# Performance work log

Hardware: AMD Instinct MI355X
Metric: run time of the kernel (lower is better)

The kernel has to match this reference:

```python
import jax, jax.numpy as jnp
import numpy as np

B, T, N, SD, D, HYP, EMB = 128, 256, 8, 200, 64, 64, 32

def _ln(x, g, b, eps=1e-5):
    mu = jnp.mean(x, -1, keepdims=True)
    v = jnp.mean((x - mu) ** 2, -1, keepdims=True)
    return (x - mu) * jax.lax.rsqrt(v + eps) * g + b

def setup_inputs():
    key = jax.random.key(0)
    ks = iter(jax.random.split(key, 64))
    def p(shape, scale=0.05):
        return (jax.random.normal(next(ks), shape) * scale).astype(jnp.float32)
    n, sd, d, hyp, emb = N, SD, D, HYP, EMB
    return dict(
        qvals=p((B, T, n), 1.0), states=p((B, T, sd), 1.0), hidden_state=p((B, T, n, d), 1.0),
        enc_w1=p((sd, d)), enc_b1=p((d,)), enc_w2=p((d, d)), enc_b2=p((d,)),
        wq=p((d, d)), bq=p((d,)), wk=p((d, d)), bk=p((d,)), wv=p((d, d)), bv=p((d,)),
        wo=p((d, d)), bo=p((d,)),
        ln1_g=jnp.ones((d,), jnp.float32), ln1_b=jnp.zeros((d,), jnp.float32),
        ffn_w1=p((d, d)), ffn_b1=p((d,)), ffn_w2=p((d, d)), ffn_b2=p((d,)),
        ln2_g=jnp.ones((d,), jnp.float32), ln2_b=jnp.zeros((d,), jnp.float32),
        fc2ni_w=p((n, d, n - 1)), fc2ni_b=p((n, n - 1)),
        norm_g=jnp.ones((n - 1,), jnp.float32), norm_b=jnp.zeros((n - 1,), jnp.float32),
        w1a=p((2 * d, hyp)), b1a=p((hyp,)), w1b=p((hyp, n * emb)), b1b=p((n * emb,)),
        hb1w=p((2 * d, emb)), hb1b=p((emb,)),
        w2a=p((2 * d, hyp)), b2a=p((hyp,)), w2b=p((hyp, emb)), b2b=p((emb,)),
        hb2w1=p((2 * d, emb)), hb2b1=p((emb,)), hb2w2=p((emb, 1)), hb2b2=p((1,)))

def reference(qvals, states, hidden_state, enc_w1, enc_b1, enc_w2, enc_b2,
              wq, bq, wk, bk, wv, bv, wo, bo, ln1_g, ln1_b,
              ffn_w1, ffn_b1, ffn_w2, ffn_b2, ln2_g, ln2_b,
              fc2ni_w, fc2ni_b, norm_g, norm_b,
              w1a, b1a, w1b, b1b, hb1w, hb1b,
              w2a, b2a, w2b, b2b, hb2w1, hb2b1, hb2w2, hb2b2):
    sg = jax.lax.stop_gradient
    b, t, n = qvals.shape
    bt = b * t
    d = hidden_state.shape[-1]
    emb = hb1w.shape[1]
    # Encoder_s: relu(fc1) then tanh(fc2(e)+e)
    s = states.reshape(bt, -1)
    e = jax.nn.relu(s @ enc_w1 + enc_b1)
    enc = jnp.tanh(e @ enc_w2 + enc_b2 + e)                       # (bt, 64)
    # concat detached agent hiddens with detached state embedding -> (bt, n+1, 64)
    h = jnp.concatenate([sg(hidden_state.reshape(bt, n, d)), sg(enc)[:, None, :]], axis=1)
    # transformer block (single-head self-attention + FFN, post-LN)
    q = h @ wq + bq; k = h @ wk + bk; v = h @ wv + bv
    att = jax.nn.softmax(jnp.einsum('bid,bjd->bij', q, k) / jnp.sqrt(jnp.float32(d)), axis=-1)
    h2 = _ln(h + (att @ v) @ wo + bo, ln1_g, ln1_b)
    h3 = _ln(h2 + jax.nn.relu(h2 @ ffn_w1 + ffn_b1) @ ffn_w2 + ffn_b2, ln2_g, ln2_b)
    h_trans = h3[:, :n]                                           # (bt, n, 64)
    ens = jnp.concatenate([enc, sg(h_trans).mean(1)], axis=-1)    # (bt, 128)
    # per-agent fc2_Ni -> LayerNorm -> sigmoid, vectorized over agents
    ni = jnp.einsum('xnd,nde->xne', h_trans, fc2ni_w) + fc2ni_b   # (bt, n, n-1)
    ni = jax.nn.sigmoid(_ln(ni, norm_g, norm_b))
    # insert 1.0 at the diagonal (agent i keeps its own q with weight 1)
    rows = jnp.arange(n)[:, None]; cols = jnp.arange(n)[None, :]
    gidx = jnp.clip(cols - (cols > rows).astype(jnp.int32), 0, n - 2)  # (n, n)
    gathered = jnp.take_along_axis(ni, jnp.broadcast_to(gidx, (bt, n, n)), axis=-1)
    nfull = jnp.where(cols == rows, jnp.float32(1.0), gathered)   # (bt, n, n)
    N_nn = nfull.reshape(b, t, n, n)
    q_ni = (qvals[:, :, None, :] * N_nn).sum(-1).reshape(bt, 1, n)
    # hypernetwork mixing (QMIX)
    ens_d = sg(ens)
    w1 = jnp.abs(jax.nn.relu(ens_d @ w1a + b1a) @ w1b + b1b).reshape(bt, n, emb)
    b1 = (ens_d @ hb1w + hb1b).reshape(bt, 1, emb)
    w2 = jnp.abs(jax.nn.relu(ens @ w2a + b2a) @ w2b + b2b).reshape(bt, emb, 1)
    b2 = (jax.nn.relu(ens @ hb2w1 + hb2b1) @ hb2w2 + hb2b2).reshape(bt, 1, 1)
    hidden = jax.nn.elu(q_ni @ w1 + b1)
    y = (hidden @ w2 + b2).reshape(b, t, 1)
    eye_mask = jnp.broadcast_to(jnp.eye(n, dtype=bool), (b, t, n, n))
    return y, N_nn, eye_mask
```

## Files before the change

### kernel.cpp

```cpp
#include <hip/hip_runtime.h>
#include <hip/hip_bf16.h>

typedef __bf16 bf16x8 __attribute__((ext_vector_type(8)));
typedef __bf16 bf16x4 __attribute__((ext_vector_type(4)));
typedef float f32x4 __attribute__((ext_vector_type(4)));

#define ROWSG 32768
#define RB 8
#define HPAD 72
#define NN_OFF ((size_t)ROWSG)
#define EYE_OFF ((size_t)ROWSG + (size_t)ROWSG*64)

#define OFF_EW1   0
#define OFF_EW2   14336
#define OFF_WQ    18432
#define OFF_WK    22528
#define OFF_WV    26624
#define OFF_WO    30720
#define OFF_F1    34816
#define OFF_F2    38912
#define OFF_W1A   43008
#define OFF_W1B   51200
#define OFF_HB1W  67584
#define OFF_W2A   71680
#define OFF_W2B   79872
#define OFF_HB2W1 81920
#define WS_TOTAL  86016

__device__ __align__(16) __bf16 g_ws[WS_TOTAL];

#define MFMA16(a,b,c) __builtin_amdgcn_mfma_f32_16x16x32_bf16(a,b,c,0,0,0)

struct TP { const float* src[14]; };

__global__ __launch_bounds__(256) void wtrans(TP tp) {
    const int gid = blockIdx.x * 256 + threadIdx.x;
    if (gid >= WS_TOTAL) return;
    const int OFFS[14] = {OFF_EW1, OFF_EW2, OFF_WQ, OFF_WK, OFF_WV, OFF_WO, OFF_F1,
                          OFF_F2, OFF_W1A, OFF_W1B, OFF_HB1W, OFF_W2A, OFF_W2B, OFF_HB2W1};
    const int KPS[14]  = {224, 64, 64, 64, 64, 64, 64, 64, 128, 64, 128, 128, 64, 128};
    const int KRS[14]  = {200, 64, 64, 64, 64, 64, 64, 64, 128, 64, 128, 128, 64, 128};
    const int NS[14]   = {64, 64, 64, 64, 64, 64, 64, 64, 64, 256, 32, 64, 32, 32};
    int m = 0;
#pragma unroll
    for (int i = 1; i < 14; ++i) if (gid >= OFFS[i]) m = i;
    const int loc = gid - OFFS[m];
    const int Kp = KPS[m];
    const int n = loc / Kp;
    const int k = loc - n * Kp;
    float v = 0.f;
    if (k < KRS[m]) v = tp.src[m][(size_t)k * NS[m] + n];
    g_ws[gid] = (__bf16)v;
}

struct MainP {
    const float *qvals, *states, *hid, *eb1, *eb2, *bq, *bk, *bv, *bo,
        *l1g, *l1b, *fb1, *fb2, *l2g, *l2b, *niw, *nib, *ng, *nb,
        *b1a, *b1b, *hb1b, *b2a, *b2b, *hb2b1, *hw2, *hb2b2;
    float* out;
};

__device__ __forceinline__ void proj_ln(const __bf16* A, const __bf16* WT,
                                        const float* bias, const float* g, const float* bb,
                                        __bf16* H, int w, int quad, int l15) {
    for (int mti = 0; mti < 2; ++mti) {
        const int mt = w + 4 * mti;
        if (mt >= 5) continue;
        f32x4 acc0 = {0,0,0,0}, acc1 = {0,0,0,0}, acc2 = {0,0,0,0}, acc3 = {0,0,0,0};
#pragma unroll
        for (int ks = 0; ks < 2; ++ks) {
            const int kk = ks * 32 + quad * 8;
            const bf16x8 af = *(const bf16x8*)(A + (mt * 16 + l15) * HPAD + kk);
            acc0 = MFMA16(af, *(const bf16x8*)(WT + (size_t)(0 * 16 + l15) * 64 + kk), acc0);
            acc1 = MFMA16(af, *(const bf16x8*)(WT + (size_t)(1 * 16 + l15) * 64 + kk), acc1);
            acc2 = MFMA16(af, *(const bf16x8*)(WT + (size_t)(2 * 16 + l15) * 64 + kk), acc2);
            acc3 = MFMA16(af, *(const bf16x8*)(WT + (size_t)(3 * 16 + l15) * 64 + kk), acc3);
        }
        float v[4][4], g4[4], b4[4];
#pragma unroll
        for (int nt = 0; nt < 4; ++nt) {
            const int col = nt * 16 + l15;
            const float bo = bias[col];
            g4[nt] = g[col]; b4[nt] = bb[col];
            const f32x4 a = (nt == 0) ? acc0 : (nt == 1) ? acc1 : (nt == 2) ? acc2 : acc3;
#pragma unroll
            for (int r = 0; r < 4; ++r)
                v[nt][r] = a[r] + bo + (float)H[(mt * 16 + quad * 4 + r) * HPAD + col];
        }
#pragma unroll
        for (int r = 0; r < 4; ++r) {
            float s  = v[0][r] + v[1][r] + v[2][r] + v[3][r];
            float s2 = v[0][r]*v[0][r] + v[1][r]*v[1][r] + v[2][r]*v[2][r] + v[3][r]*v[3][r];
#pragma unroll
            for (int off = 1; off < 16; off <<= 1) {
                s  += __shfl_xor(s,  off, 64);
                s2 += __shfl_xor(s2, off, 64);
            }
            const float mu  = s * 0.015625f;
            const float var = s2 * 0.015625f - mu * mu;
            const float rs  = rsqrtf(var + 1e-5f);
#pragma unroll
            for (int nt = 0; nt < 4; ++nt)
                H[(mt * 16 + quad * 4 + r) * HPAD + nt * 16 + l15] =
                    (__bf16)((v[nt][r] - mu) * rs * g4[nt] + b4[nt]);
        }
    }
}

__global__ __launch_bounds__(256) void mixer_main(MainP p) {
    __shared__ __align__(16) __bf16 Hb[80 * HPAD];
    __shared__ __align__(16) __bf16 Qb[80 * HPAD];
    __shared__ __align__(16) __bf16 Kb[80 * HPAD];
    __shared__ __align__(16) __bf16 EbU[16 * HPAD];
    __shared__ __align__(16) __bf16 Tb2[16 * HPAD];
    __shared__ __align__(16) __bf16 ensB[16 * 136];
    __shared__ float  attU[8 * 81];
    __shared__ float  sQv[64];
    __shared__ float  qniL[64];
    __shared__ __align__(16) __bf16 W1bS[8 * 256];
    __shared__ float  B1f[8 * 32], W2f[8 * 32], T3f[8 * 32];

    const int blk = blockIdx.x;
    const int bt0 = blk * RB;
    const int t = threadIdx.x;
    const int w = t >> 6, lane = t & 63, quad = lane >> 4, l15 = lane & 15;
    const __bf16* ws = g_ws;
    __bf16* Sb = W1bS;

#pragma unroll
    for (int it = 0; it < 4; ++it) {
        const int u = it * 256 + t;
        const int x = u >> 7, rem = u & 127, n = rem >> 4, d4 = (rem & 15) * 4;
        const float4 v4 = *(const float4*)(p.hid + ((size_t)(bt0 + x) * 512 + n * 64 + d4));
        bf16x4 o; o[0] = (__bf16)v4.x; o[1] = (__bf16)v4.y; o[2] = (__bf16)v4.z; o[3] = (__bf16)v4.w;
        *(bf16x4*)(Hb + (x * 9 + n) * HPAD + d4) = o;
    }
#pragma unroll
    for (int it = 0; it < 2; ++it) {
        const int u = it * 256 + t;
        if (u < 400) {
            const int xr = u / 50, c4 = u - xr * 50;
            const float4 v4 = *(const float4*)(p.states + (size_t)(bt0 + xr) * 200 + c4 * 4);
            bf16x4 o; o[0] = (__bf16)v4.x; o[1] = (__bf16)v4.y; o[2] = (__bf16)v4.z; o[3] = (__bf16)v4.w;
            *(bf16x4*)(Sb + xr * 224 + c4 * 4) = o;
        }
    }
    if (t < 192) { const int xr = t / 24, c = t - xr * 24; Sb[xr * 224 + 200 + c] = (__bf16)0.0f; }
    if (t < 64) sQv[t] = p.qvals[(size_t)(bt0 + (t >> 3)) * 8 + (t & 7)];
    __syncthreads();

    float e4[4];
    {
        const int n0 = w * 16;
        const int srow = (l15 < 8) ? l15 : 7;
        f32x4 acc = {0, 0, 0, 0};
        for (int ks = 0; ks < 7; ++ks) {
            const int kk = ks * 32 + quad * 8;
            const bf16x8 af = *(const bf16x8*)(Sb + srow * 224 + kk);
            const bf16x8 bf = *(const bf16x8*)(ws + OFF_EW1 + (size_t)(n0 + l15) * 224 + kk);
            acc = MFMA16(af, bf, acc);
        }
        const float b1 = p.eb1[n0 + l15];
#pragma unroll
        for (int r = 0; r < 4; ++r) {
            const float ev = fmaxf(acc[r] + b1, 0.f);
            e4[r] = ev;
            EbU[(quad * 4 + r) * HPAD + n0 + l15] = (__bf16)ev;
        }
    }
    __syncthreads();

    {
        const int n0 = w * 16;
        f32x4 acc = {0, 0, 0, 0};
#pragma unroll
        for (int ks = 0; ks < 2; ++ks) {
            const int kk = ks * 32 + quad * 8;
            const bf16x8 af = *(const bf16x8*)(EbU + l15 * HPAD + kk);
            const bf16x8 bf = *(const bf16x8*)(ws + OFF_EW2 + (size_t)(n0 + l15) * 64 + kk);
            acc = MFMA16(af, bf, acc);
        }
        const float b2 = p.eb2[n0 + l15];
#pragma unroll
        for (int r = 0; r < 4; ++r) {
            const int xr = quad * 4 + r;
            if (xr < RB) {
                const float ev = tanhf(acc[r] + e4[r] + b2);
                Hb[(xr * 9 + 8) * HPAD + n0 + l15] = (__bf16)ev;
                ensB[xr * 136 + n0 + l15] = (__bf16)ev;
            }
        }
    }
    __syncthreads();

    for (int it = 0; it < 10; ++it) {
        const int j = w + 4 * it;
        const int mat = j / 20, r20 = j % 20, mt = r20 >> 2, nt = r20 & 3;
        const __bf16* wt = ws + (mat == 0 ? OFF_WQ : OFF_WK);
        const float* bias = (mat == 0 ? p.bq : p.bk);
        __bf16* dst = (mat == 0 ? Qb : Kb);
        f32x4 acc = {0, 0, 0, 0};
#pragma unroll
        for (int ks = 0; ks < 2; ++ks) {
            const int kk = ks * 32 + quad * 8;
            const bf16x8 af = *(const bf16x8*)(Hb + (mt * 16 + l15) * HPAD + kk);
            const bf16x8 bf = *(const bf16x8*)(wt + (size_t)(nt * 16 + l15) * 64 + kk);
            acc = MFMA16(af, bf, acc);
        }
        const float bv = bias[nt * 16 + l15];
#pragma unroll
        for (int r = 0; r < 4; ++r)
            dst[(mt * 16 + quad * 4 + r) * HPAD + nt * 16 + l15] = (__bf16)(acc[r] + bv);
    }
    __syncthreads();

    for (int xi = 0; xi < 2; ++xi) {
        const int x = w * 2 + xi;
        const int arow = (x * 9 + l15) * HPAD;
        f32x4 acc = {0, 0, 0, 0};
#pragma unroll
        for (int ks = 0; ks < 2; ++ks) {
            const int kk = ks * 32 + quad * 8;
            const bf16x8 qa = *(const bf16x8*)(Qb + arow + kk);
            const bf16x8 kb = *(const bf16x8*)(Kb + arow + kk);
            acc = MFMA16(qa, kb, acc);
        }
#pragma unroll
        for (int r = 0; r < 4; ++r) {
            const int i = quad * 4 + r;
            float s = (l15 < 9) ? acc[r] * 0.125f : -3.0e38f;
            float m = s;
#pragma unroll
            for (int off = 1; off < 16; off <<= 1) m = fmaxf(m, __shfl_xor(m, off, 64));
            float e = (l15 < 9) ? __expf(s - m) : 0.f;
            float sum = e;
#pragma unroll
            for (int off = 1; off < 16; off <<= 1) sum += __shfl_xor(sum, off, 64);
            const float pv = e / sum;
            if (i < 9 && l15 < 9) attU[x * 81 + i * 9 + l15] = pv;
        }
    }
    __syncthreads();

    for (int xi = 0; xi < 2; ++xi) {
        const int x = w * 2 + xi;
        float vreg[9];
#pragma unroll
        for (int jj = 0; jj < 9; ++jj) vreg[jj] = (float)Hb[(x * 9 + jj) * HPAD + lane];
#pragma unroll
        for (int i = 0; i < 9; ++i) {
            float a = 0.f;
#pragma unroll
            for (int jj = 0; jj < 9; ++jj) a += attU[x * 81 + i * 9 + jj] * vreg[jj];
            Kb[(x * 9 + i) * HPAD + lane] = (__bf16)a;
        }
    }
    __syncthreads();

    for (int it = 0; it < 5; ++it) {
        const int j = w + 4 * it;
        const int mt = j >> 2, nt = j & 3;
        f32x4 acc = {0, 0, 0, 0};
#pragma unroll
        for (int ks = 0; ks < 2; ++ks) {
            const int kk = ks * 32 + quad * 8;
            const bf16x8 af = *(const bf16x8*)(Kb + (mt * 16 + l15) * HPAD + kk);
            const bf16x8 bf = *(const bf16x8*)(ws + OFF_WV + (size_t)(nt * 16 + l15) * 64 + kk);
            acc = MFMA16(af, bf, acc);
        }
        const float bv = p.bv[nt * 16 + l15];
#pragma unroll
        for (int r = 0; r < 4; ++r)
            Qb[(mt * 16 + quad * 4 + r) * HPAD + nt * 16 + l15] = (__bf16)(acc[r] + bv);
    }
    __syncthreads();

    proj_ln(Qb, ws + OFF_WO, p.bo, p.l1g, p.l1b, Hb, w, quad, l15);
    __syncthreads();

    for (int it = 0; it < 5; ++it) {
        const int j = w + 4 * it;
        const int mt = j >> 2, nt = j & 3;
        f32x4 acc = {0, 0, 0, 0};
#pragma unroll
        for (int ks = 0; ks < 2; ++ks) {
            const int kk = ks * 32 + quad * 8;
            const bf16x8 af = *(const bf16x8*)(Hb + (mt * 16 + l15) * HPAD + kk);
            const bf16x8 bf = *(const bf16x8*)(ws + OFF_F1 + (size_t)(nt * 16 + l15) * 64 + kk);
            acc = MFMA16(af, bf, acc);
        }
        const float fb = p.fb1[nt * 16 + l15];
#pragma unroll
        for (int r = 0; r < 4; ++r)
            Kb[(mt * 16 + quad * 4 + r) * HPAD + nt * 16 + l15] = (__bf16)fmaxf(acc[r] + fb, 0.f);
    }
    __syncthreads();

    proj_ln(Kb, ws + OFF_F2, p.fb2, p.l2g, p.l2b, Hb, w, quad, l15);
    __syncthreads();

#pragma unroll
    for (int it = 0; it < 2; ++it) {
        const int id = it * 256 + t;
        const int x = id >> 6, col = id & 63;
        float s = 0.f;
#pragma unroll
        for (int i = 0; i < 8; ++i) s += (float)Hb[(x * 9 + i) * HPAD + col];
        ensB[x * 136 + 64 + col] = (__bf16)(s * 0.125f);
    }
    __syncthreads();

    {
        const int pr = t >> 2, q4 = t & 3;
        const int x = pr >> 3, n = pr & 7;
        float acc[7] = {0.f, 0.f, 0.f, 0.f, 0.f, 0.f, 0.f};
        const float* wni = p.niw + n * 448;
        for (int dd = 0; dd < 16; ++dd) {
            const int d = q4 * 16 + dd;
            const float hv = (float)Hb[(x * 9 + n) * HPAD + d];
#pragma unroll
            for (int e = 0; e < 7; ++e) acc[e] += hv * wni[d * 7 + e];
        }
#pragma unroll
        for (int e = 0; e < 7; ++e) {
            acc[e] += __shfl_xor(acc[e], 1, 64);
            acc[e] += __shfl_xor(acc[e], 2, 64);
        }
        if (q4 == 0) {
            float s = 0.f;
#pragma unroll
            for (int e = 0; e < 7; ++e) { acc[e] += p.nib[n * 7 + e]; s += acc[e]; }
            const float mu = s * (1.f / 7.f);
            float s2 = 0.f;
#pragma unroll
            for (int e = 0; e < 7; ++e) { const float d0 = acc[e] - mu; s2 += d0 * d0; }
            const float rs = rsqrtf(s2 * (1.f / 7.f) + 1e-5f);
            float* sNi = (float*)EbU;
#pragma unroll
            for (int e = 0; e < 7; ++e) {
                const float vv = (acc[e] - mu) * rs * p.ng[e] + p.nb[e];
                sNi[x * 64 + n * 8 + e] = 1.f / (1.f + __expf(-vv));
            }
        }
    }
    __syncthreads();

    {
        const float* sNi = (const float*)EbU;
        float* Nf = attU;
#pragma unroll
        for (int it = 0; it < 2; ++it) {
            const int id = it * 256 + t;
            const int x = id >> 6, rem = id & 63, i = rem >> 3, jj = rem & 7;
            const float nf = (i == jj) ? 1.f : sNi[x * 64 + i * 8 + (jj - (jj > i ? 1 : 0))];
            p.out[NN_OFF + (size_t)(bt0 + x) * 64 + rem] = nf;
            p.out[EYE_OFF + (size_t)(bt0 + x) * 64 + rem] = (i == jj) ? 1.f : 0.f;
            Nf[x * 64 + rem] = nf;
        }
    }
    __syncthreads();
    {
        const float* Nf = attU;
        const int pr = t >> 2, q4 = t & 3;
        const int x = pr >> 3, i = pr & 7;
        const int j0 = q4 * 2;
        float s = sQv[x * 8 + j0] * Nf[x * 64 + i * 8 + j0] +
                  sQv[x * 8 + j0 + 1] * Nf[x * 64 + i * 8 + j0 + 1];
        s += __shfl_xor(s, 1, 64);
        s += __shfl_xor(s, 2, 64);
        if (q4 == 0) qniL[x * 8 + i] = s;
    }
    __syncthreads();

    {
        const int n0 = w * 16;
#pragma unroll
        for (int m2 = 0; m2 < 2; ++m2) {
            const __bf16* wt = ws + (m2 == 0 ? OFF_W1A : OFF_W2A);
            const float* bias = m2 == 0 ? p.b1a : p.b2a;
            __bf16* dst = m2 == 0 ? EbU : Tb2;
            f32x4 acc = {0, 0, 0, 0};
#pragma unroll
            for (int ks = 0; ks < 4; ++ks) {
                const int kk = ks * 32 + quad * 8;
                const bf16x8 af = *(const bf16x8*)(ensB + l15 * 136 + kk);
                const bf16x8 bf = *(const bf16x8*)(wt + (size_t)(n0 + l15) * 128 + kk);
                acc = MFMA16(af, bf, acc);
            }
            const float bb = bias[n0 + l15];
#pragma unroll
            for (int r = 0; r < 4; ++r)
                dst[(quad * 4 + r) * HPAD + n0 + l15] = (__bf16)fmaxf(acc[r] + bb, 0.f);
        }
    }
    __syncthreads();

    for (int it = 0; it < 6; ++it) {
        const int j = w + 4 * it;
        if (j >= 22) continue;
        int mode, n0, Kp, ksteps, aStride;
        const __bf16 *A, *WT; const float* bias;
        if (j < 16)      { mode = 0; n0 = j * 16;        A = EbU;  aStride = HPAD; WT = ws + OFF_W1B;   bias = p.b1b;  Kp = 64;  ksteps = 2; }
        else if (j < 18) { mode = 1; n0 = (j - 16) * 16; A = ensB; aStride = 136;  WT = ws + OFF_HB1W;  bias = p.hb1b; Kp = 128; ksteps = 4; }
        else if (j < 20) { mode = 2; n0 = (j - 18) * 16; A = Tb2;  aStride = HPAD; WT = ws + OFF_W2B;   bias = p.b2b;  Kp = 64;  ksteps = 2; }
        else             { mode = 3; n0 = (j - 20) * 16; A = ensB; aStride = 136;  WT = ws + OFF_HB2W1; bias = p.hb2b1;Kp = 128; ksteps = 4; }
        f32x4 acc = {0, 0, 0, 0};
        for (int ks = 0; ks < ksteps; ++ks) {
            const int kk = ks * 32 + quad * 8;
            const bf16x8 af = *(const bf16x8*)(A + l15 * aStride + kk);
            const bf16x8 bf = *(const bf16x8*)(WT + (size_t)(n0 + l15) * Kp + kk);
            acc = MFMA16(af, bf, acc);
        }
        const float bb = bias[n0 + l15];
#pragma unroll
        for (int r = 0; r < 4; ++r) {
            const int xr = quad * 4 + r;
            if (xr < RB) {
                const float val = acc[r] + bb;
                if (mode == 0)      W1bS[xr * 256 + n0 + l15] = (__bf16)fabsf(val);
                else if (mode == 1) B1f[xr * 32 + n0 + l15] = val;
                else if (mode == 2) W2f[xr * 32 + n0 + l15] = fabsf(val);
                else                T3f[xr * 32 + n0 + l15] = fmaxf(val, 0.f);
            }
        }
    }
    __syncthreads();

    if (t < 128) {
        const int x = t >> 4, sub = t & 15;
        float pp = 0.f, pb = 0.f;
#pragma unroll
        for (int h2i = 0; h2i < 2; ++h2i) {
            const int e = sub + h2i * 16;
            float a = B1f[x * 32 + e];
#pragma unroll
            for (int i = 0; i < 8; ++i) a += qniL[x * 8 + i] * (float)W1bS[x * 256 + i * 32 + e];
            const float hid = a > 0.f ? a : (__expf(a) - 1.f);
            pp += hid * W2f[x * 32 + e];
            pb += T3f[x * 32 + e] * p.hw2[e];
        }
#pragma unroll
        for (int off = 1; off < 16; off <<= 1) {
            pp += __shfl_xor(pp, off, 64);
            pb += __shfl_xor(pb, off, 64);
        }
        if (sub == 0) p.out[bt0 + x] = pp + pb + p.hb2b2[0];
    }
}

extern "C" void kernel_launch(void* const* d_in, const int* in_sizes, int n_in,
                              void* d_out, int out_size, void* d_ws, size_t ws_size,
                              hipStream_t stream) {
    TP tp;
    tp.src[0]  = (const float*)d_in[3];
    tp.src[1]  = (const float*)d_in[5];
    tp.src[2]  = (const float*)d_in[7];
    tp.src[3]  = (const float*)d_in[9];
    tp.src[4]  = (const float*)d_in[11];
    tp.src[5]  = (const float*)d_in[13];
    tp.src[6]  = (const float*)d_in[17];
    tp.src[7]  = (const float*)d_in[19];
    tp.src[8]  = (const float*)d_in[27];
    tp.src[9]  = (const float*)d_in[29];
    tp.src[10] = (const float*)d_in[31];
    tp.src[11] = (const float*)d_in[33];
    tp.src[12] = (const float*)d_in[35];
    tp.src[13] = (const float*)d_in[37];
    wtrans<<<(WS_TOTAL + 255) / 256, 256, 0, stream>>>(tp);

    MainP p;
    p.qvals = (const float*)d_in[0];
    p.states = (const float*)d_in[1];
    p.hid = (const float*)d_in[2];
    p.eb1 = (const float*)d_in[4];
    p.eb2 = (const float*)d_in[6];
    p.bq = (const float*)d_in[8];
    p.bk = (const float*)d_in[10];
    p.bv = (const float*)d_in[12];
    p.bo = (const float*)d_in[14];
    p.l1g = (const float*)d_in[15];
    p.l1b = (const float*)d_in[16];
    p.fb1 = (const float*)d_in[18];
    p.fb2 = (const float*)d_in[20];
    p.l2g = (const float*)d_in[21];
    p.l2b = (const float*)d_in[22];
    p.niw = (const float*)d_in[23];
    p.nib = (const float*)d_in[24];
    p.ng = (const float*)d_in[25];
    p.nb = (const float*)d_in[26];
    p.b1a = (const float*)d_in[28];
    p.b1b = (const float*)d_in[30];
    p.hb1b = (const float*)d_in[32];
    p.b2a = (const float*)d_in[34];
    p.b2b = (const float*)d_in[36];
    p.hb2b1 = (const float*)d_in[38];
    p.hw2 = (const float*)d_in[39];
    p.hb2b2 = (const float*)d_in[40];
    p.out = (float*)d_out;

    mixer_main<<<ROWSG / RB, 256, 0, stream>>>(p);
}
```

Before: 430.8 us.

## Give each wavefront its own rows and LDS slice to drop block barriers

Restructures the fused mixer kernel so each of the four wavefronts processes two batch-time rows independently in a private 8 KB LDS slice, removing all block-wide __syncthreads. Per-row work (attention over 9 tokens, FFN, layer norms, hypernetwork heads) now uses MFMA tiles with only 9 of 16 rows valid, trading wasted MFMA lanes for no inter-wave synchronisation. It also cuts shared memory and adds a launch bound of 4 blocks per CU to raise occupancy. The risks are lower MFMA utilisation, since more tiles are padded, and weight reloads now happen per wave rather than once per block.

```diff
diff --git a/kernel.cpp b/kernel.cpp
--- a/kernel.cpp
+++ b/kernel.cpp
@@ -6,8 +6,6 @@
 typedef float f32x4 __attribute__((ext_vector_type(4)));
 
 #define ROWSG 32768
-#define RB 8
-#define HPAD 72
 #define NN_OFF ((size_t)ROWSG)
 #define EYE_OFF ((size_t)ROWSG + (size_t)ROWSG*64)
 
@@ -60,391 +58,391 @@
     float* out;
 };
 
-__device__ __forceinline__ void proj_ln(const __bf16* A, const __bf16* WT,
-                                        const float* bias, const float* g, const float* bb,
-                                        __bf16* H, int w, int quad, int l15) {
-    for (int mti = 0; mti < 2; ++mti) {
-        const int mt = w + 4 * mti;
-        if (mt >= 5) continue;
-        f32x4 acc0 = {0,0,0,0}, acc1 = {0,0,0,0}, acc2 = {0,0,0,0}, acc3 = {0,0,0,0};
+__device__ __forceinline__ void proj_ln_row(const __bf16* A, const __bf16* WT,
+                                            const float* bias, const float* g, const float* bb,
+                                            __bf16* H, int quad, int l15) {
+    f32x4 acc[4] = {{0,0,0,0},{0,0,0,0},{0,0,0,0},{0,0,0,0}};
+#pragma unroll
+    for (int ks = 0; ks < 2; ++ks) {
+        const int kk = ks * 32 + quad * 8;
+        const bf16x8 af = *(const bf16x8*)(A + l15 * 72 + kk);
+#pragma unroll
+        for (int nt = 0; nt < 4; ++nt)
+            acc[nt] = MFMA16(af, *(const bf16x8*)(WT + (size_t)(nt * 16 + l15) * 64 + kk), acc[nt]);
+    }
+    float v[4][4], g4[4], b4[4];
+#pragma unroll
+    for (int nt = 0; nt < 4; ++nt) {
+        const int col = nt * 16 + l15;
+        const float bo = bias[col];
+        g4[nt] = g[col]; b4[nt] = bb[col];
+#pragma unroll
+        for (int r = 0; r < 4; ++r)
+            v[nt][r] = acc[nt][r] + bo + (float)H[(quad * 4 + r) * 72 + col];
+    }
+#pragma unroll
+    for (int r = 0; r < 4; ++r) {
+        float s  = v[0][r] + v[1][r] + v[2][r] + v[3][r];
+        float s2 = v[0][r]*v[0][r] + v[1][r]*v[1][r] + v[2][r]*v[2][r] + v[3][r]*v[3][r];
+#pragma unroll
+        for (int off = 1; off < 16; off <<= 1) {
+            s  += __shfl_xor(s,  off, 64);
+            s2 += __shfl_xor(s2, off, 64);
+        }
+        const float mu  = s * 0.015625f;
+        const float var = s2 * 0.015625f - mu * mu;
+        const float rs  = rsqrtf(var + 1e-5f);
+        const int i = quad * 4 + r;
+        if (i < 9) {
+#pragma unroll
+            for (int nt = 0; nt < 4; ++nt)
+                H[i * 72 + nt * 16 + l15] = (__bf16)((v[nt][r] - mu) * rs * g4[nt] + b4[nt]);
+        }
+    }
+}
+
+__global__ __launch_bounds__(256, 4) void mixer_main(MainP p) {
+    __shared__ __align__(16) unsigned char LDSraw[4 * 8192];
+
+    const int t = threadIdx.x;
+    const int w = t >> 6, lane = t & 63, quad = lane >> 4, l15 = lane & 15;
+    const int r0 = blockIdx.x * 8 + w * 2;
+    const __bf16* ws = g_ws;
+
+    unsigned char* SLICE = LDSraw + w * 8192;
+    __bf16* T = (__bf16*)SLICE;
+    unsigned char* SC = SLICE + 4896;
+    __bf16* Sb   = (__bf16*)(SC + 0);
+    float*  attP = (float*) (SC + 0);
+    float*  sNi  = (float*) (SC + 448);
+    __bf16* W1s  = (__bf16*)(SC + 0);
+    __bf16* Eb   = (__bf16*)(SC + 896);
+    __bf16* ENC  = (__bf16*)(SC + 1152);
+    __bf16* ENS  = (__bf16*)(SC + 1408);
+    __bf16* T1   = (__bf16*)(SC + 1920);
+    __bf16* T2   = (__bf16*)(SC + 2176);
+    float*  QNI  = (float*) (SC + 2432);
+    float*  B1f  = (float*) (SC + 2496);
+    float*  W2f  = (float*) (SC + 2752);
+    float*  T3f  = (float*) (SC + 3008);
+
+    for (int it = 0; it < 7; ++it) {
+        const int u = it * 64 + lane;
+        if (u < 448) {
+            const int rr = (u >= 224) ? 1 : 0;
+            const int c = u - rr * 224;
+            float v = 0.f;
+            if (c < 200) v = p.states[(size_t)(r0 + rr) * 200 + c];
+            Sb[rr * 224 + c] = (__bf16)v;
+        }
+    }
+
+    float er[2][4];
+    {
+        const int arow = (l15 & 1) * 224;
+        f32x4 acc[4] = {{0,0,0,0},{0,0,0,0},{0,0,0,0},{0,0,0,0}};
+        for (int ks = 0; ks < 7; ++ks) {
+            const int kk = ks * 32 + quad * 8;
+            const bf16x8 af = *(const bf16x8*)(Sb + arow + kk);
+#pragma unroll
+            for (int nt = 0; nt < 4; ++nt)
+                acc[nt] = MFMA16(af, *(const bf16x8*)(ws + OFF_EW1 + (size_t)(nt * 16 + l15) * 224 + kk), acc[nt]);
+        }
+#pragma unroll
+        for (int nt = 0; nt < 4; ++nt) {
+            const float b1 = p.eb1[nt * 16 + l15];
+#pragma unroll
+            for (int r = 0; r < 2; ++r) {
+                const float ev = fmaxf(acc[nt][r] + b1, 0.f);
+                er[r][nt] = ev;
+                if (quad == 0) Eb[r * 64 + nt * 16 + l15] = (__bf16)ev;
+            }
+        }
+    }
+
+    {
+        const int arow = (l15 & 1) * 64;
+        f32x4 acc[4] = {{0,0,0,0},{0,0,0,0},{0,0,0,0},{0,0,0,0}};
 #pragma unroll
         for (int ks = 0; ks < 2; ++ks) {
             const int kk = ks * 32 + quad * 8;
-            const bf16x8 af = *(const bf16x8*)(A + (mt * 16 + l15) * HPAD + kk);
-            acc0 = MFMA16(af, *(const bf16x8*)(WT + (size_t)(0 * 16 + l15) * 64 + kk), acc0);
-            acc1 = MFMA16(af, *(const bf16x8*)(WT + (size_t)(1 * 16 + l15) * 64 + kk), acc1);
-            acc2 = MFMA16(af, *(const bf16x8*)(WT + (size_t)(2 * 16 + l15) * 64 + kk), acc2);
-            acc3 = MFMA16(af, *(const bf16x8*)(WT + (size_t)(3 * 16 + l15) * 64 + kk), acc3);
-        }
-        float v[4][4], g4[4], b4[4];
-#pragma unroll
-        for (int nt = 0; nt < 4; ++nt) {
-            const int col = nt * 16 + l15;
-            const float bo = bias[col];
-            g4[nt] = g[col]; b4[nt] = bb[col];
-            const f32x4 a = (nt == 0) ? acc0 : (nt == 1) ? acc1 : (nt == 2) ? acc2 : acc3;
-#pragma unroll
-            for (int r = 0; r < 4; ++r)
-                v[nt][r] = a[r] + bo + (float)H[(mt * 16 + quad * 4 + r) * HPAD + col];
-        }
-#pragma unroll
-        for (int r = 0; r < 4; ++r) {
-            float s  = v[0][r] + v[1][r] + v[2][r] + v[3][r];
-            float s2 = v[0][r]*v[0][r] + v[1][r]*v[1][r] + v[2][r]*v[2][r] + v[3][r]*v[3][r];
-#pragma unroll
-            for (int off = 1; off < 16; off <<= 1) {
-                s  += __shfl_xor(s,  off, 64);
-                s2 += __shfl_xor(s2, off, 64);
-            }
-            const float mu  = s * 0.015625f;
-            const float var = s2 * 0.015625f - mu * mu;
-            const float rs  = rsqrtf(var + 1e-5f);
+            const bf16x8 af = *(const bf16x8*)(Eb + arow + kk);
 #pragma unroll
             for (int nt = 0; nt < 4; ++nt)
-                H[(mt * 16 + quad * 4 + r) * HPAD + nt * 16 + l15] =
-                    (__bf16)((v[nt][r] - mu) * rs * g4[nt] + b4[nt]);
-        }
-    }
-}
-
-__global__ __launch_bounds__(256) void mixer_main(MainP p) {
-    __shared__ __align__(16) __bf16 Hb[80 * HPAD];
-    __shared__ __align__(16) __bf16 Qb[80 * HPAD];
-    __shared__ __align__(16) __bf16 Kb[80 * HPAD];
-    __shared__ __align__(16) __bf16 EbU[16 * HPAD];
-    __shared__ __align__(16) __bf16 Tb2[16 * HPAD];
-    __shared__ __align__(16) __bf16 ensB[16 * 136];
-    __shared__ float  attU[8 * 81];
-    __shared__ float  sQv[64];
-    __shared__ float  qniL[64];
-    __shared__ __align__(16) __bf16 W1bS[8 * 256];
-    __shared__ float  B1f[8 * 32], W2f[8 * 32], T3f[8 * 32];
-
-    const int blk = blockIdx.x;
-    const int bt0 = blk * RB;
-    const int t = threadIdx.x;
-    const int w = t >> 6, lane = t & 63, quad = lane >> 4, l15 = lane & 15;
-    const __bf16* ws = g_ws;
-    __bf16* Sb = W1bS;
-
-#pragma unroll
-    for (int it = 0; it < 4; ++it) {
-        const int u = it * 256 + t;
-        const int x = u >> 7, rem = u & 127, n = rem >> 4, d4 = (rem & 15) * 4;
-        const float4 v4 = *(const float4*)(p.hid + ((size_t)(bt0 + x) * 512 + n * 64 + d4));
-        bf16x4 o; o[0] = (__bf16)v4.x; o[1] = (__bf16)v4.y; o[2] = (__bf16)v4.z; o[3] = (__bf16)v4.w;
-        *(bf16x4*)(Hb + (x * 9 + n) * HPAD + d4) = o;
-    }
-#pragma unroll
-    for (int it = 0; it < 2; ++it) {
-        const int u = it * 256 + t;
-        if (u < 400) {
-            const int xr = u / 50, c4 = u - xr * 50;
-            const float4 v4 = *(const float4*)(p.states + (size_t)(bt0 + xr) * 200 + c4 * 4);
+                acc[nt] = MFMA16(af, *(const bf16x8*)(ws + OFF_EW2 + (size_t)(nt * 16 + l15) * 64 + kk), acc[nt]);
+        }
+        if (quad == 0) {
+#pragma unroll
+            for (int nt = 0; nt < 4; ++nt) {
+                const float b2 = p.eb2[nt * 16 + l15];
+#pragma unroll
+                for (int r = 0; r < 2; ++r)
+                    ENC[r * 64 + nt * 16 + l15] = (__bf16)tanhf(acc[nt][r] + er[r][nt] + b2);
+            }
+        }
+    }
+
+    for (int xi = 0; xi < 2; ++xi) {
+        const int bt = r0 + xi;
+
+#pragma unroll
+        for (int it = 0; it < 2; ++it) {
+            const int u = it * 64 + lane;
+            const int n = u >> 4, c4 = (u & 15) * 4;
+            const float4 v4 = *(const float4*)(p.hid + ((size_t)bt * 8 + n) * 64 + c4);
             bf16x4 o; o[0] = (__bf16)v4.x; o[1] = (__bf16)v4.y; o[2] = (__bf16)v4.z; o[3] = (__bf16)v4.w;
-            *(bf16x4*)(Sb + xr * 224 + c4 * 4) = o;
-        }
-    }
-    if (t < 192) { const int xr = t / 24, c = t - xr * 24; Sb[xr * 224 + 200 + c] = (__bf16)0.0f; }
-    if (t < 64) sQv[t] = p.qvals[(size_t)(bt0 + (t >> 3)) * 8 + (t & 7)];
-    __syncthreads();
-
-    float e4[4];
-    {
-        const int n0 = w * 16;
-        const int srow = (l15 < 8) ? l15 : 7;
-        f32x4 acc = {0, 0, 0, 0};
-        for (int ks = 0; ks < 7; ++ks) {
+            *(bf16x4*)(T + n * 72 + c4) = o;
+        }
+        T[8 * 72 + lane] = ENC[xi * 64 + lane];
+
+#pragma unroll
+        for (int mat = 0; mat < 2; ++mat) {
+            const __bf16* wt = ws + (mat == 0 ? OFF_WQ : OFF_WK);
+            const float* bias = mat == 0 ? p.bq : p.bk;
+            const int rbase = mat == 0 ? 9 : 18;
+            f32x4 acc[4] = {{0,0,0,0},{0,0,0,0},{0,0,0,0},{0,0,0,0}};
+#pragma unroll
+            for (int ks = 0; ks < 2; ++ks) {
+                const int kk = ks * 32 + quad * 8;
+                const bf16x8 af = *(const bf16x8*)(T + l15 * 72 + kk);
+#pragma unroll
+                for (int nt = 0; nt < 4; ++nt)
+                    acc[nt] = MFMA16(af, *(const bf16x8*)(wt + (size_t)(nt * 16 + l15) * 64 + kk), acc[nt]);
+            }
+#pragma unroll
+            for (int nt = 0; nt < 4; ++nt) {
+                const float bv = bias[nt * 16 + l15];
+#pragma unroll
+                for (int r = 0; r < 4; ++r) {
+                    const int i = quad * 4 + r;
+                    if (i < 9) T[(rbase + i) * 72 + nt * 16 + l15] = (__bf16)(acc[nt][r] + bv);
+                }
+            }
+        }
+
+        {
+            f32x4 acc = {0, 0, 0, 0};
+#pragma unroll
+            for (int ks = 0; ks < 2; ++ks) {
+                const int kk = ks * 32 + quad * 8;
+                const bf16x8 qa = *(const bf16x8*)(T + (9 + l15) * 72 + kk);
+                const bf16x8 kb = *(const bf16x8*)(T + (18 + l15) * 72 + kk);
+                acc = MFMA16(qa, kb, acc);
+            }
+#pragma unroll
+            for (int r = 0; r < 4; ++r) {
+                const int i = quad * 4 + r;
+                float s = (l15 < 9) ? acc[r] * 0.125f : -3.0e38f;
+                float m = s;
+#pragma unroll
+                for (int off = 1; off < 16; off <<= 1) m = fmaxf(m, __shfl_xor(m, off, 64));
+                float e = (l15 < 9) ? __expf(s - m) : 0.f;
+                float sum = e;
+#pragma unroll
+                for (int off = 1; off < 16; off <<= 1) sum += __shfl_xor(sum, off, 64);
+                if (i < 9 && l15 < 9) attP[i * 9 + l15] = e / sum;
+            }
+        }
+
+        {
+            float vreg[9];
+#pragma unroll
+            for (int j = 0; j < 9; ++j) vreg[j] = (float)T[j * 72 + lane];
+#pragma unroll
+            for (int i = 0; i < 9; ++i) {
+                float a = 0.f;
+#pragma unroll
+                for (int j = 0; j < 9; ++j) a += attP[i * 9 + j] * vreg[j];
+                T[(9 + i) * 72 + lane] = (__bf16)a;
+            }
+        }
+
+        {
+            f32x4 acc[4] = {{0,0,0,0},{0,0,0,0},{0,0,0,0},{0,0,0,0}};
+#pragma unroll
+            for (int ks = 0; ks < 2; ++ks) {
+                const int kk = ks * 32 + quad * 8;
+                const bf16x8 af = *(const bf16x8*)(T + (9 + l15) * 72 + kk);
+#pragma unroll
+                for (int nt = 0; nt < 4; ++nt)
+                    acc[nt] = MFMA16(af, *(const bf16x8*)(ws + OFF_WV + (size_t)(nt * 16 + l15) * 64 + kk), acc[nt]);
+            }
+#pragma unroll
+            for (int nt = 0; nt < 4; ++nt) {
+                const float bv = p.bv[nt * 16 + l15];
+#pragma unroll
+                for (int r = 0; r < 4; ++r) {
+                    const int i = quad * 4 + r;
+                    if (i < 9) T[(18 + i) * 72 + nt * 16 + l15] = (__bf16)(acc[nt][r] + bv);
+                }
+            }
+        }
+
+        proj_ln_row(T + 18 * 72, ws + OFF_WO, p.bo, p.l1g, p.l1b, T, quad, l15);
+
+        {
+            f32x4 acc[4] = {{0,0,0,0},{0,0,0,0},{0,0,0,0},{0,0,0,0}};
+#pragma unroll
+            for (int ks = 0; ks < 2; ++ks) {
+                const int kk = ks * 32 + quad * 8;
+                const bf16x8 af = *(const bf16x8*)(T + l15 * 72 + kk);
+#pragma unroll
+                for (int nt = 0; nt < 4; ++nt)
+                    acc[nt] = MFMA16(af, *(const bf16x8*)(ws + OFF_F1 + (size_t)(nt * 16 + l15) * 64 + kk), acc[nt]);
+            }
+#pragma unroll
+            for (int nt = 0; nt < 4; ++nt) {
+                const float fb = p.fb1[nt * 16 + l15];
+#pragma unroll
+                for (int r = 0; r < 4; ++r) {
+                    const int i = quad * 4 + r;
+                    if (i < 9) T[(9 + i) * 72 + nt * 16 + l15] = (__bf16)fmaxf(acc[nt][r] + fb, 0.f);
+                }
+            }
+        }
+
+        proj_ln_row(T + 9 * 72, ws + OFF_F2, p.fb2, p.l2g, p.l2b, T, quad, l15);
+
+        {
+            const int n = lane >> 3, e = lane & 7;
+            float acc = 0.f;
+            if (e < 7) {
+                const float* wni = p.niw + n * 448 + e;
+#pragma unroll
+                for (int d8 = 0; d8 < 8; ++d8) {
+                    const bf16x8 hv = *(const bf16x8*)(T + n * 72 + d8 * 8);
+#pragma unroll
+                    for (int q2 = 0; q2 < 8; ++q2)
+                        acc += (float)hv[q2] * wni[(d8 * 8 + q2) * 7];
+                }
+                acc += p.nib[n * 7 + e];
+            }
+            float s1 = (e < 7) ? acc : 0.f;
+            s1 += __shfl_xor(s1, 1, 64); s1 += __shfl_xor(s1, 2, 64); s1 += __shfl_xor(s1, 4, 64);
+            const float mu = s1 * (1.f / 7.f);
+            float d0 = (e < 7) ? (acc - mu) : 0.f;
+            float s2 = d0 * d0;
+            s2 += __shfl_xor(s2, 1, 64); s2 += __shfl_xor(s2, 2, 64); s2 += __shfl_xor(s2, 4, 64);
+            const float rs = rsqrtf(s2 * (1.f / 7.f) + 1e-5f);
+            if (e < 7) {
+                const float vv = (acc - mu) * rs * p.ng[e] + p.nb[e];
+                sNi[n * 7 + e] = 1.f / (1.f + __expf(-vv));
+            }
+        }
+
+        {
+            const int i = lane >> 3, j = lane & 7;
+            const float nf = (i == j) ? 1.f : sNi[i * 7 + j - (j > i ? 1 : 0)];
+            p.out[NN_OFF + (size_t)bt * 64 + lane] = nf;
+            p.out[EYE_OFF + (size_t)bt * 64 + lane] = (i == j) ? 1.f : 0.f;
+            float s = p.qvals[(size_t)bt * 8 + j] * nf;
+            s += __shfl_xor(s, 1, 64); s += __shfl_xor(s, 2, 64); s += __shfl_xor(s, 4, 64);
+            if (j == 0) QNI[xi * 8 + i] = s;
+        }
+
+        {
+            float m = 0.f;
+#pragma unroll
+            for (int n = 0; n < 8; ++n) m += (float)T[n * 72 + lane];
+            ENS[xi * 128 + lane] = ENC[xi * 64 + lane];
+            ENS[xi * 128 + 64 + lane] = (__bf16)(m * 0.125f);
+        }
+    }
+
+#pragma unroll
+    for (int m2 = 0; m2 < 2; ++m2) {
+        const __bf16* wt = ws + (m2 == 0 ? OFF_W1A : OFF_W2A);
+        const float* bias = m2 == 0 ? p.b1a : p.b2a;
+        __bf16* dst = m2 == 0 ? T1 : T2;
+        f32x4 acc[4] = {{0,0,0,0},{0,0,0,0},{0,0,0,0},{0,0,0,0}};
+#pragma unroll
+        for (int ks = 0; ks < 4; ++ks) {
             const int kk = ks * 32 + quad * 8;
-            const bf16x8 af = *(const bf16x8*)(Sb + srow * 224 + kk);
-            const bf16x8 bf = *(const bf16x8*)(ws + OFF_EW1 + (size_t)(n0 + l15) * 224 + kk);
-            acc = MFMA16(af, bf, acc);
-        }
-        const float b1 = p.eb1[n0 + l15];
-#pragma unroll
-        for (int r = 0; r < 4; ++r) {
-            const float ev = fmaxf(acc[r] + b1, 0.f);
-            e4[r] = ev;
-            EbU[(quad * 4 + r) * HPAD + n0 + l15] = (__bf16)ev;
-        }
-    }
-    __syncthreads();
-
-    {
-        const int n0 = w * 16;
-        f32x4 acc = {0, 0, 0, 0};
+            const bf16x8 af = *(const bf16x8*)(ENS + (l15 & 1) * 128 + kk);
+#pragma unroll
+            for (int nt = 0; nt < 4; ++nt)
+                acc[nt] = MFMA16(af, *(const bf16x8*)(wt + (size_t)(nt * 16 + l15) * 128 + kk), acc[nt]);
+        }
+        if (quad == 0) {
+#pragma unroll
+            for (int nt = 0; nt < 4; ++nt) {
+                const float bb = bias[nt * 16 + l15];
+#pragma unroll
+                for (int r = 0; r < 2; ++r)
+                    dst[r * 64 + nt * 16 + l15] = (__bf16)fmaxf(acc[nt][r] + bb, 0.f);
+            }
+        }
+    }
+#pragma unroll
+    for (int g4i = 0; g4i < 4; ++g4i) {
+        f32x4 acc[4] = {{0,0,0,0},{0,0,0,0},{0,0,0,0},{0,0,0,0}};
 #pragma unroll
         for (int ks = 0; ks < 2; ++ks) {
             const int kk = ks * 32 + quad * 8;
-            const bf16x8 af = *(const bf16x8*)(EbU + l15 * HPAD + kk);
-            const bf16x8 bf = *(const bf16x8*)(ws + OFF_EW2 + (size_t)(n0 + l15) * 64 + kk);
-            acc = MFMA16(af, bf, acc);
-        }
-        const float b2 = p.eb2[n0 + l15];
-#pragma unroll
-        for (int r = 0; r < 4; ++r) {
-            const int xr = quad * 4 + r;
-            if (xr < RB) {
-                const float ev = tanhf(acc[r] + e4[r] + b2);
-                Hb[(xr * 9 + 8) * HPAD + n0 + l15] = (__bf16)ev;
-                ensB[xr * 136 + n0 + l15] = (__bf16)ev;
-            }
-        }
-    }
-    __syncthreads();
-
-    for (int it = 0; it < 10; ++it) {
-        const int j = w + 4 * it;
-        const int mat = j / 20, r20 = j % 20, mt = r20 >> 2, nt = r20 & 3;
-        const __bf16* wt = ws + (mat == 0 ? OFF_WQ : OFF_WK);
-        const float* bias = (mat == 0 ? p.bq : p.bk);
-        __bf16* dst = (mat == 0 ? Qb : Kb);
-        f32x4 acc = {0, 0, 0, 0};
+            const bf16x8 af = *(const bf16x8*)(T1 + (l15 & 1) * 64 + kk);
+#pragma unroll
+            for (int nt = 0; nt < 4; ++nt) {
+                const int n0 = (g4i * 4 + nt) * 16;
+                acc[nt] = MFMA16(af, *(const bf16x8*)(ws + OFF_W1B + (size_t)(n0 + l15) * 64 + kk), acc[nt]);
+            }
+        }
+        if (quad == 0) {
+#pragma unroll
+            for (int nt = 0; nt < 4; ++nt) {
+                const int n0 = (g4i * 4 + nt) * 16;
+                const float bb = p.b1b[n0 + l15];
+#pragma unroll
+                for (int r = 0; r < 2; ++r)
+                    W1s[r * 256 + n0 + l15] = (__bf16)fabsf(acc[nt][r] + bb);
+            }
+        }
+    }
+    {
+        f32x4 accB[2] = {{0,0,0,0},{0,0,0,0}};
+        f32x4 accT[2] = {{0,0,0,0},{0,0,0,0}};
+        f32x4 accW[2] = {{0,0,0,0},{0,0,0,0}};
+#pragma unroll
+        for (int ks = 0; ks < 4; ++ks) {
+            const int kk = ks * 32 + quad * 8;
+            const bf16x8 af = *(const bf16x8*)(ENS + (l15 & 1) * 128 + kk);
+#pragma unroll
+            for (int nt = 0; nt < 2; ++nt) {
+                accB[nt] = MFMA16(af, *(const bf16x8*)(ws + OFF_HB1W  + (size_t)(nt * 16 + l15) * 128 + kk), accB[nt]);
+                accT[nt] = MFMA16(af, *(const bf16x8*)(ws + OFF_HB2W1 + (size_t)(nt * 16 + l15) * 128 + kk), accT[nt]);
+            }
+        }
 #pragma unroll
         for (int ks = 0; ks < 2; ++ks) {
             const int kk = ks * 32 + quad * 8;
-            const bf16x8 af = *(const bf16x8*)(Hb + (mt * 16 + l15) * HPAD + kk);
-            const bf16x8 bf = *(const bf16x8*)(wt + (size_t)(nt * 16 + l15) * 64 + kk);
-            acc = MFMA16(af, bf, acc);
-        }
-        const float bv = bias[nt * 16 + l15];
-#pragma unroll
-        for (int r = 0; r < 4; ++r)
-            dst[(mt * 16 + quad * 4 + r) * HPAD + nt * 16 + l15] = (__bf16)(acc[r] + bv);
-    }
-    __syncthreads();
-
-    for (int xi = 0; xi < 2; ++xi) {
-        const int x = w * 2 + xi;
-        const int arow = (x * 9 + l15) * HPAD;
-        f32x4 acc = {0, 0, 0, 0};
-#pragma unroll
-        for (int ks = 0; ks < 2; ++ks) {
-            const int kk = ks * 32 + quad * 8;
-            const bf16x8 qa = *(const bf16x8*)(Qb + arow + kk);
-            const bf16x8 kb = *(const bf16x8*)(Kb + arow + kk);
-            acc = MFMA16(qa, kb, acc);
-        }
-#pragma unroll
-        for (int r = 0; r < 4; ++r) {
-            const int i = quad * 4 + r;
-            float s = (l15 < 9) ? acc[r] * 0.125f : -3.0e38f;
-            float m = s;
-#pragma unroll
-            for (int off = 1; off < 16; off <<= 1) m = fmaxf(m, __shfl_xor(m, off, 64));
-            float e = (l15 < 9) ? __expf(s - m) : 0.f;
-            float sum = e;
-#pragma unroll
-            for (int off = 1; off < 16; off <<= 1) sum += __shfl_xor(sum, off, 64);
-            const float pv = e / sum;
-            if (i < 9 && l15 < 9) attU[x * 81 + i * 9 + l15] = pv;
-        }
-    }
-    __syncthreads();
-
-    for (int xi = 0; xi < 2; ++xi) {
-        const int x = w * 2 + xi;
-        float vreg[9];
-#pragma unroll
-        for (int jj = 0; jj < 9; ++jj) vreg[jj] = (float)Hb[(x * 9 + jj) * HPAD + lane];
-#pragma unroll
-        for (int i = 0; i < 9; ++i) {
-            float a = 0.f;
-#pragma unroll
-            for (int jj = 0; jj < 9; ++jj) a += attU[x * 81 + i * 9 + jj] * vreg[jj];
-            Kb[(x * 9 + i) * HPAD + lane] = (__bf16)a;
-        }
-    }
-    __syncthreads();
-
-    for (int it = 0; it < 5; ++it) {
-        const int j = w + 4 * it;
-        const int mt = j >> 2, nt = j & 3;
-        f32x4 acc = {0, 0, 0, 0};
-#pragma unroll
-        for (int ks = 0; ks < 2; ++ks) {
-            const int kk = ks * 32 + quad * 8;
-            const bf16x8 af = *(const bf16x8*)(Kb + (mt * 16 + l15) * HPAD + kk);
-            const bf16x8 bf = *(const bf16x8*)(ws + OFF_WV + (size_t)(nt * 16 + l15) * 64 + kk);
-            acc = MFMA16(af, bf, acc);
-        }
-        const float bv = p.bv[nt * 16 + l15];
-#pragma unroll
-        for (int r = 0; r < 4; ++r)
-            Qb[(mt * 16 + quad * 4 + r) * HPAD + nt * 16 + l15] = (__bf16)(acc[r] + bv);
-    }
-    __syncthreads();
-
-    proj_ln(Qb, ws + OFF_WO, p.bo, p.l1g, p.l1b, Hb, w, quad, l15);
-    __syncthreads();
-
-    for (int it = 0; it < 5; ++it) {
-        const int j = w + 4 * it;
-        const int mt = j >> 2, nt = j & 3;
-        f32x4 acc = {0, 0, 0, 0};
-#pragma unroll
-        for (int ks = 0; ks < 2; ++ks) {
-            const int kk = ks * 32 + quad * 8;
-            const bf16x8 af = *(const bf16x8*)(Hb + (mt * 16 + l15) * HPAD + kk);
-            const bf16x8 bf = *(const bf16x8*)(ws + OFF_F1 + (size_t)(nt * 16 + l15) * 64 + kk);
-            acc = MFMA16(af, bf, acc);
-        }
-        const float fb = p.fb1[nt * 16 + l15];
-#pragma unroll
-        for (int r = 0; r < 4; ++r)
-            Kb[(mt * 16 + quad * 4 + r) * HPAD + nt * 16 + l15] = (__bf16)fmaxf(acc[r] + fb, 0.f);
-    }
-    __syncthreads();
-
-    proj_ln(Kb, ws + OFF_F2, p.fb2, p.l2g, p.l2b, Hb, w, quad, l15);
-    __syncthreads();
-
-#pragma unroll
-    for (int it = 0; it < 2; ++it) {
-        const int id = it * 256 + t;
-        const int x = id >> 6, col = id & 63;
-        float s = 0.f;
-#pragma unroll
-        for (int i = 0; i < 8; ++i) s += (float)Hb[(x * 9 + i) * HPAD + col];
-        ensB[x * 136 + 64 + col] = (__bf16)(s * 0.125f);
-    }
-    __syncthreads();
-
+            const bf16x8 af = *(const bf16x8*)(T2 + (l15 & 1) * 64 + kk);
+#pragma unroll
+            for (int nt = 0; nt < 2; ++nt)
+                accW[nt] = MFMA16(af, *(const bf16x8*)(ws + OFF_W2B + (size_t)(nt * 16 + l15) * 64 + kk), accW[nt]);
+        }
+        if (quad == 0) {
+#pragma unroll
+            for (int nt = 0; nt < 2; ++nt) {
+                const int c = nt * 16 + l15;
+                const float bB = p.hb1b[c], bT = p.hb2b1[c], bW = p.b2b[c];
+#pragma unroll
+                for (int r = 0; r < 2; ++r) {
+                    B1f[r * 32 + c] = accB[nt][r] + bB;
+                    T3f[r * 32 + c] = fmaxf(accT[nt][r] + bT, 0.f);
+                    W2f[r * 32 + c] = fabsf(accW[nt][r] + bW);
+                }
+            }
+        }
+    }
     {
-        const int pr = t >> 2, q4 = t & 3;
-        const int x = pr >> 3, n = pr & 7;
-        float acc[7] = {0.f, 0.f, 0.f, 0.f, 0.f, 0.f, 0.f};
-        const float* wni = p.niw + n * 448;
-        for (int dd = 0; dd < 16; ++dd) {
-            const int d = q4 * 16 + dd;
-            const float hv = (float)Hb[(x * 9 + n) * HPAD + d];
-#pragma unroll
-            for (int e = 0; e < 7; ++e) acc[e] += hv * wni[d * 7 + e];
-        }
-#pragma unroll
-        for (int e = 0; e < 7; ++e) {
-            acc[e] += __shfl_xor(acc[e], 1, 64);
-            acc[e] += __shfl_xor(acc[e], 2, 64);
-        }
-        if (q4 == 0) {
-            float s = 0.f;
-#pragma unroll
-            for (int e = 0; e < 7; ++e) { acc[e] += p.nib[n * 7 + e]; s += acc[e]; }
-            const float mu = s * (1.f / 7.f);
-            float s2 = 0.f;
-#pragma unroll
-            for (int e = 0; e < 7; ++e) { const float d0 = acc[e] - mu; s2 += d0 * d0; }
-            const float rs = rsqrtf(s2 * (1.f / 7.f) + 1e-5f);
-            float* sNi = (float*)EbU;
-#pragma unroll
-            for (int e = 0; e < 7; ++e) {
-                const float vv = (acc[e] - mu) * rs * p.ng[e] + p.nb[e];
-                sNi[x * 64 + n * 8 + e] = 1.f / (1.f + __expf(-vv));
-            }
-        }
-    }
-    __syncthreads();
-
-    {
-        const float* sNi = (const float*)EbU;
-        float* Nf = attU;
-#pragma unroll
-        for (int it = 0; it < 2; ++it) {
-            const int id = it * 256 + t;
-            const int x = id >> 6, rem = id & 63, i = rem >> 3, jj = rem & 7;
-            const float nf = (i == jj) ? 1.f : sNi[x * 64 + i * 8 + (jj - (jj > i ? 1 : 0))];
-            p.out[NN_OFF + (size_t)(bt0 + x) * 64 + rem] = nf;
-            p.out[EYE_OFF + (size_t)(bt0 + x) * 64 + rem] = (i == jj) ? 1.f : 0.f;
-            Nf[x * 64 + rem] = nf;
-        }
-    }
-    __syncthreads();
-    {
-        const float* Nf = attU;
-        const int pr = t >> 2, q4 = t & 3;
-        const int x = pr >> 3, i = pr & 7;
-        const int j0 = q4 * 2;
-        float s = sQv[x * 8 + j0] * Nf[x * 64 + i * 8 + j0] +
-                  sQv[x * 8 + j0 + 1] * Nf[x * 64 + i * 8 + j0 + 1];
-        s += __shfl_xor(s, 1, 64);
-        s += __shfl_xor(s, 2, 64);
-        if (q4 == 0) qniL[x * 8 + i] = s;
-    }
-    __syncthreads();
-
-    {
-        const int n0 = w * 16;
-#pragma unroll
-        for (int m2 = 0; m2 < 2; ++m2) {
-            const __bf16* wt = ws + (m2 == 0 ? OFF_W1A : OFF_W2A);
-            const float* bias = m2 == 0 ? p.b1a : p.b2a;
-            __bf16* dst = m2 == 0 ? EbU : Tb2;
-            f32x4 acc = {0, 0, 0, 0};
-#pragma unroll
-            for (int ks = 0; ks < 4; ++ks) {
-                const int kk = ks * 32 + quad * 8;
-                const bf16x8 af = *(const bf16x8*)(ensB + l15 * 136 + kk);
-                const bf16x8 bf = *(const bf16x8*)(wt + (size_t)(n0 + l15) * 128 + kk);
-                acc = MFMA16(af, bf, acc);
-            }
-            const float bb = bias[n0 + l15];
-#pragma unroll
-            for (int r = 0; r < 4; ++r)
-                dst[(quad * 4 + r) * HPAD + n0 + l15] = (__bf16)fmaxf(acc[r] + bb, 0.f);
-        }
-    }
-    __syncthreads();
-
-    for (int it = 0; it < 6; ++it) {
-        const int j = w + 4 * it;
-        if (j >= 22) continue;
-        int mode, n0, Kp, ksteps, aStride;
-        const __bf16 *A, *WT; const float* bias;
-        if (j < 16)      { mode = 0; n0 = j * 16;        A = EbU;  aStride = HPAD; WT = ws + OFF_W1B;   bias = p.b1b;  Kp = 64;  ksteps = 2; }
-        else if (j < 18) { mode = 1; n0 = (j - 16) * 16; A = ensB; aStride = 136;  WT = ws + OFF_HB1W;  bias = p.hb1b; Kp = 128; ksteps = 4; }
-        else if (j < 20) { mode = 2; n0 = (j - 18) * 16; A = Tb2;  aStride = HPAD; WT = ws + OFF_W2B;   bias = p.b2b;  Kp = 64;  ksteps = 2; }
-        else             { mode = 3; n0 = (j - 20) * 16; A = ensB; aStride = 136;  WT = ws + OFF_HB2W1; bias = p.hb2b1;Kp = 128; ksteps = 4; }
-        f32x4 acc = {0, 0, 0, 0};
-        for (int ks = 0; ks < ksteps; ++ks) {
-            const int kk = ks * 32 + quad * 8;
-            const bf16x8 af = *(const bf16x8*)(A + l15 * aStride + kk);
-            const bf16x8 bf = *(const bf16x8*)(WT + (size_t)(n0 + l15) * Kp + kk);
-            acc = MFMA16(af, bf, acc);
-        }
-        const float bb = bias[n0 + l15];
-#pragma unroll
-        for (int r = 0; r < 4; ++r) {
-            const int xr = quad * 4 + r;
-            if (xr < RB) {
-                const float val = acc[r] + bb;
-                if (mode == 0)      W1bS[xr * 256 + n0 + l15] = (__bf16)fabsf(val);
-                else if (mode == 1) B1f[xr * 32 + n0 + l15] = val;
-                else if (mode == 2) W2f[xr * 32 + n0 + l15] = fabsf(val);
-                else                T3f[xr * 32 + n0 + l15] = fmaxf(val, 0.f);
-            }
-        }
-    }
-    __syncthreads();
-
-    if (t < 128) {
-        const int x = t >> 4, sub = t & 15;
-        float pp = 0.f, pb = 0.f;
-#pragma unroll
-        for (int h2i = 0; h2i < 2; ++h2i) {
-            const int e = sub + h2i * 16;
-            float a = B1f[x * 32 + e];
-#pragma unroll
-            for (int i = 0; i < 8; ++i) a += qniL[x * 8 + i] * (float)W1bS[x * 256 + i * 32 + e];
-            const float hid = a > 0.f ? a : (__expf(a) - 1.f);
-            pp += hid * W2f[x * 32 + e];
-            pb += T3f[x * 32 + e] * p.hw2[e];
-        }
-#pragma unroll
-        for (int off = 1; off < 16; off <<= 1) {
-            pp += __shfl_xor(pp, off, 64);
-            pb += __shfl_xor(pb, off, 64);
-        }
-        if (sub == 0) p.out[bt0 + x] = pp + pb + p.hb2b2[0];
+        const int xr = lane >> 5, e = lane & 31;
+        float a = B1f[xr * 32 + e];
+#pragma unroll
+        for (int i = 0; i < 8; ++i) a += QNI[xr * 8 + i] * (float)W1s[xr * 256 + i * 32 + e];
+        const float hid = a > 0.f ? a : (__expf(a) - 1.f);
+        float pp = hid * W2f[xr * 32 + e] + T3f[xr * 32 + e] * p.hw2[e];
+#pragma unroll
+        for (int off = 1; off < 32; off <<= 1) pp += __shfl_xor(pp, off, 64);
+        if (e == 0) p.out[(size_t)(r0 + xr)] = pp + p.hb2b2[0];
     }
 }
 
@@ -498,5 +496,5 @@
     p.hb2b2 = (const float*)d_in[40];
     p.out = (float*)d_out;
 
-    mixer_main<<<ROWSG / RB, 256, 0, stream>>>(p);
+    mixer_main<<<ROWSG / 8, 256, 0, stream>>>(p);
 }
```

After: 819.0 us. +90.1%, slower.
